# Performance work log

Hardware: AMD Instinct MI355X
Metric: run time of the kernel (lower is better)

Reference implementation:

```python
import jax, jax.numpy as jnp
import numpy as np

D_MODEL = 512
NUM_HEADS = 8
D_K = D_MODEL // NUM_HEADS


def setup_inputs() -> dict:
    key = jax.random.key(0)
    k0, k1, k2, k3, k4 = jax.random.split(key, 5)
    s = 1.0 / np.sqrt(D_MODEL)
    return {
        "x": jax.random.normal(k0, (2, 4096, D_MODEL), dtype=jnp.float32),
        "W_q": jax.random.normal(k1, (D_MODEL, D_MODEL), dtype=jnp.float32) * s,
        "W_k": jax.random.normal(k2, (D_MODEL, D_MODEL), dtype=jnp.float32) * s,
        "W_v": jax.random.normal(k3, (D_MODEL, D_MODEL), dtype=jnp.float32) * s,
        "W_o": jax.random.normal(k4, (D_MODEL, D_MODEL), dtype=jnp.float32) * s,
    }


def reference(x, W_q, W_k, W_v, W_o):
    B, S, _ = x.shape
    # project and split heads: (B, H, S, d_k)
    def split(t):
        return t.reshape(B, S, NUM_HEADS, D_K).transpose(0, 2, 1, 3)
    Q = split(x @ W_q)
    K = split(x @ W_k)
    V = split(x @ W_v)
    scale = jnp.sqrt(jnp.asarray(D_K, dtype=x.dtype))
    logits = jnp.einsum('bhqd,bhkd->bhqk', Q, K) / scale
    attn = jax.nn.softmax(logits, axis=-1)  # dropout is identity at inference
    out = jnp.einsum('bhqk,bhkd->bhqd', attn, V)
    concat = out.transpose(0, 2, 1, 3).reshape(B, S, D_MODEL)
    return concat @ W_o
```

## Files before the change

kernel.cpp:

```cpp
#include <hip/hip_runtime.h>
#include <hip/hip_bf16.h>


#define DMODEL 512
#define SEQ    4096
#define NTOK   8192
#define LDQK   1024

using f32x4 = __attribute__((ext_vector_type(4))) float;
using s16x8 = __attribute__((ext_vector_type(8))) short;
using u16x8 = __attribute__((ext_vector_type(8))) unsigned short;

static __device__ __forceinline__ unsigned short f2bf(float f) {
  union { float f; unsigned u; } v; v.f = f;
  unsigned r = v.u + 0x7fff + ((v.u >> 16) & 1);
  return (unsigned short)(r >> 16);
}

static __device__ __forceinline__ unsigned pack_bf2(float lo, float hi) {
  __hip_bfloat162 t = __float22bfloat162_rn(make_float2(lo, hi));
  union { __hip_bfloat162 b; unsigned u; } c; c.b = t; return c.u;
}

static __device__ __forceinline__ void gll16(const void* g, void* l) {
  __builtin_amdgcn_global_load_lds(
      (const __attribute__((address_space(1))) unsigned int*)g,
      (__attribute__((address_space(3))) unsigned int*)l, 16, 0, 0);
}

__global__ void prep_kernel(const float* __restrict__ x,
                            const float* __restrict__ Wq,
                            const float* __restrict__ Wk,
                            const float* __restrict__ Wv,
                            const float* __restrict__ Wo,
                            unsigned short* __restrict__ xb,
                            unsigned short* __restrict__ Wall, float c2) {
  __shared__ float T[64][65];
  const int bx = blockIdx.x;
  if (bx < 1024) {
    for (int i = bx * 256 + threadIdx.x; i < NTOK * DMODEL / 4; i += 262144) {
      float4 v = ((const float4*)x)[i];
      ushort4 o;
      o.x = f2bf(v.x); o.y = f2bf(v.y); o.z = f2bf(v.z); o.w = f2bf(v.w);
      ((ushort4*)xb)[i] = o;
    }
    return;
  }
  const int t = bx - 1024;
  const int y = t >> 6, sub = t & 63;
  const float* W = (y == 0) ? Wq : (y == 1) ? Wk : (y == 2) ? Wv : Wo;
  const float scale = (y == 0) ? c2 : 1.0f;
  const int tk = (sub & 7) * 64;
  const int tn = (sub >> 3) * 64;
  const int r  = threadIdx.x >> 2;
  const int cq = threadIdx.x & 3;
#pragma unroll
  for (int i = 0; i < 4; ++i) {
    int c = (cq + 4 * i) * 4;
    float4 v = *(const float4*)&W[(size_t)(tk + r) * 512 + tn + c];
    T[r][c + 0] = v.x * scale; T[r][c + 1] = v.y * scale;
    T[r][c + 2] = v.z * scale; T[r][c + 3] = v.w * scale;
  }
  __syncthreads();
  const int n  = threadIdx.x >> 2;
  const int k0 = (threadIdx.x & 3) * 16;
#pragma unroll
  for (int j4 = 0; j4 < 4; ++j4) {
    ushort4 o;
    o.x = f2bf(T[k0 + j4 * 4 + 0][n]);
    o.y = f2bf(T[k0 + j4 * 4 + 1][n]);
    o.z = f2bf(T[k0 + j4 * 4 + 2][n]);
    o.w = f2bf(T[k0 + j4 * 4 + 3][n]);
    *(ushort4*)&Wall[(size_t)y * 262144 + (size_t)(tn + n) * 512 + tk + k0 + j4 * 4] = o;
  }
}

__global__ __launch_bounds__(256, 3) void gemm_qkv(
    const unsigned short* __restrict__ xb,
    const unsigned short* __restrict__ Wall,
    unsigned short* __restrict__ QKb,
    unsigned short* __restrict__ Vtb)
{
  __shared__ unsigned short As[128 * 32];
  __shared__ unsigned short Bs[128 * 32];
  const int by = blockIdx.y;
  const bool vmode = (by >= 8);
  const unsigned short* A  = vmode ? (Wall + 2 * 262144) : xb;
  const unsigned short* Bt = vmode ? xb : Wall;
  const size_t bm = vmode ? (size_t)(by - 8) * 128 : (size_t)blockIdx.x * 128;
  const size_t bn = vmode ? (size_t)blockIdx.x * 128 : (size_t)by * 128;
  const int tid  = threadIdx.x;
  const int wave = tid >> 6, lane = tid & 63;
  const int q4 = lane >> 4, ln = lane & 15;
  const int wm = (wave >> 1) * 64, wn = (wave & 1) * 64;
  f32x4 acc[4][4] = {};
  const int srow = wave * 16 + (lane >> 2);
  const int scol = (lane & 3) * 8;

  const unsigned short* Ag  = A  + (bm + srow)      * 512 + scol;
  const unsigned short* Ag2 = A  + (bm + 64 + srow) * 512 + scol;
  const unsigned short* Bg  = Bt + (bn + srow)      * 512 + scol;
  const unsigned short* Bg2 = Bt + (bn + 64 + srow) * 512 + scol;
  unsigned short* Ad  = As + wave * 512;
  unsigned short* Ad2 = As + 2048 + wave * 512;
  unsigned short* Bd  = Bs + wave * 512;
  unsigned short* Bd2 = Bs + 2048 + wave * 512;

  for (int kt = 0; kt < 512; kt += 32) {
    __syncthreads();
    gll16(Ag + kt,  Ad);
    gll16(Ag2 + kt, Ad2);
    gll16(Bg + kt,  Bd);
    gll16(Bg2 + kt, Bd2);
    __syncthreads();
    s16x8 af[4], bfr[4];
#pragma unroll
    for (int i = 0; i < 4; i++)
      af[i] = *(const s16x8*)(As + (wm + i * 16 + ln) * 32 + q4 * 8);
#pragma unroll
    for (int i = 0; i < 4; i++)
      bfr[i] = *(const s16x8*)(Bs + (wn + i * 16 + ln) * 32 + q4 * 8);
#pragma unroll
    for (int mi = 0; mi < 4; mi++)
#pragma unroll
      for (int ni = 0; ni < 4; ni++)
        acc[mi][ni] = __builtin_amdgcn_mfma_f32_16x16x32_bf16(
            af[mi], bfr[ni], acc[mi][ni], 0, 0, 0);
  }
#pragma unroll
  for (int mi = 0; mi < 4; mi++)
#pragma unroll
    for (int r = 0; r < 4; ++r) {
      size_t row = bm + wm + mi * 16 + q4 * 4 + r;
#pragma unroll
      for (int ni = 0; ni < 4; ni++) {
        size_t col = bn + wn + ni * 16 + ln;
        unsigned short hv = f2bf(acc[mi][ni][r]);
        if (!vmode) {
          QKb[row * 1024 + col] = hv;
        } else {
          int b = (int)(col >> 12), s = (int)(col & 4095);
          int sp = (s & ~63) | (s & 32) | (((s >> 2) & 3) << 3) |
                   (((s >> 4) & 1) << 2) | (s & 3);
          Vtb[(size_t)b * 2097152 + row * 4096 + sp] = hv;
        }
      }
    }
}

__global__ __launch_bounds__(256, 2) void attn_kernel(
    const unsigned short* __restrict__ QK,
    const unsigned short* __restrict__ Vt,
    unsigned short* __restrict__ Oc)
{
  const int bid = blockIdx.x + 32 * (blockIdx.y + 8 * blockIdx.z);
  const int lin = (bid & 7) * 64 + (bid >> 3);
  const int qt = lin & 31, bh = lin >> 5;
  const int h = bh & 7, b = bh >> 3;
  const int tid = threadIdx.x, wave = tid >> 6, lane = tid & 63;
  const int q4 = lane >> 4, ln = lane & 15;
  __shared__ unsigned short Ks[2][64 * 64];
  __shared__ unsigned short Vs[2][64 * 64];
  const size_t rowbase = (size_t)b * SEQ;
  const size_t qrow0   = (size_t)qt * 128 + wave * 32;
  const unsigned short* Kp  = QK + rowbase * LDQK + 512 + h * 64;
  const unsigned short* VTp = Vt + ((size_t)(b * 8 + h) * 64) * SEQ;

  s16x8 qf[2][2];
#pragma unroll
  for (int mf = 0; mf < 2; ++mf) {
    const unsigned short* q = QK + (rowbase + qrow0 + mf * 16 + ln) * LDQK + h * 64;
    qf[mf][0] = *(const s16x8*)(q + q4 * 8);
    qf[mf][1] = *(const s16x8*)(q + 32 + q4 * 8);
  }
  f32x4 o[2][4] = {};
  float lp[2] = {};

  const int srow = tid >> 2;
  const int c32  = (tid & 3) * 32;
  const int swz  = (srow & 7) << 4;
  const int wof0 = srow * 128 + ((c32 +  0) ^ swz);
  const int wof1 = srow * 128 + ((c32 + 16) ^ swz);
  const int rswz = (ln & 7) << 4;

  const unsigned short* kgp = Kp  + (size_t)srow * LDQK + (c32 >> 1);
  const unsigned short* vgp = VTp + (size_t)srow * SEQ + (c32 >> 1);

  u16x8 kr  = *(const u16x8*)kgp;
  u16x8 kr2 = *(const u16x8*)(kgp + 8);
  u16x8 vr  = *(const u16x8*)vgp;
  u16x8 vr2 = *(const u16x8*)(vgp + 8);
  *(u16x8*)((char*)Ks[0] + wof0) = kr;
  *(u16x8*)((char*)Ks[0] + wof1) = kr2;
  *(u16x8*)((char*)Vs[0] + wof0) = vr;
  *(u16x8*)((char*)Vs[0] + wof1) = vr2;
  kgp += (size_t)64 * LDQK;  vgp += 64;
  kr  = *(const u16x8*)kgp;
  kr2 = *(const u16x8*)(kgp + 8);
  vr  = *(const u16x8*)vgp;
  vr2 = *(const u16x8*)(vgp + 8);
  __syncthreads();

  const f32x4 fz = {0.f, 0.f, 0.f, 0.f};

  s16x8 vfp[2][4];
  s16x8 pfp[2][2];

  {
    const char* Kc = (const char*)Ks[0];
    const char* Vc = (const char*)Vs[0];
    f32x4 s4[2][4];
#pragma unroll
    for (int ni = 0; ni < 4; ni++) {
      const char* kb = Kc + (ni * 16 + ln) * 128;
      s16x8 kf0 = *(const s16x8*)(kb + ((q4 * 16)      ^ rswz));
      s16x8 kf1 = *(const s16x8*)(kb + ((q4 * 16 + 64) ^ rswz));
      __builtin_amdgcn_s_setprio(1);
#pragma unroll
      for (int mf = 0; mf < 2; ++mf) {
        f32x4 acc0 = __builtin_amdgcn_mfma_f32_16x16x32_bf16(kf0, qf[mf][0], fz, 0, 0, 0);
        s4[mf][ni] = __builtin_amdgcn_mfma_f32_16x16x32_bf16(kf1, qf[mf][1], acc0, 0, 0, 0);
      }
      __builtin_amdgcn_s_setprio(0);
    }
#pragma unroll
    for (int ks = 0; ks < 2; ++ks)
#pragma unroll
      for (int ni = 0; ni < 4; ni++)
        vfp[ks][ni] = *(const s16x8*)(Vc + (ni * 16 + ln) * 128 +
                                      ((ks * 64 + q4 * 16) ^ rswz));
#pragma unroll
    for (int mf = 0; mf < 2; ++mf) {
      float e[4][4];
#pragma unroll
      for (int ni = 0; ni < 4; ni++)
#pragma unroll
        for (int r = 0; r < 4; ++r)
          e[ni][r] = __builtin_amdgcn_exp2f(s4[mf][ni][r]);
      float t0 = (e[0][0] + e[0][1]) + (e[0][2] + e[0][3]);
      float t1 = (e[1][0] + e[1][1]) + (e[1][2] + e[1][3]);
      float t2 = (e[2][0] + e[2][1]) + (e[2][2] + e[2][3]);
      float t3 = (e[3][0] + e[3][1]) + (e[3][2] + e[3][3]);
      lp[mf] += (t0 + t1) + (t2 + t3);
#pragma unroll
      for (int ks = 0; ks < 2; ++ks) {
        union { s16x8 v; unsigned u[4]; } pu;
        pu.u[0] = pack_bf2(e[2 * ks][0],     e[2 * ks][1]);
        pu.u[1] = pack_bf2(e[2 * ks][2],     e[2 * ks][3]);
        pu.u[2] = pack_bf2(e[2 * ks + 1][0], e[2 * ks + 1][1]);
        pu.u[3] = pack_bf2(e[2 * ks + 1][2], e[2 * ks + 1][3]);
        pfp[mf][ks] = pu.v;
      }
    }
    char* Kn = (char*)Ks[1];
    char* Vn = (char*)Vs[1];
    *(u16x8*)(Kn + wof0) = kr;
    *(u16x8*)(Kn + wof1) = kr2;
    *(u16x8*)(Vn + wof0) = vr;
    *(u16x8*)(Vn + wof1) = vr2;
    kgp += (size_t)64 * LDQK;  vgp += 64;
    kr  = *(const u16x8*)kgp;
    kr2 = *(const u16x8*)(kgp + 8);
    vr  = *(const u16x8*)vgp;
    vr2 = *(const u16x8*)(vgp + 8);
    __syncthreads();
  }

  for (int t = 1; t < 64; ++t) {
    const int cur = t & 1;
    const char* Kc = (const char*)Ks[cur];
    const char* Vc = (const char*)Vs[cur];

    f32x4 s4[2][4];
#pragma unroll
    for (int ni = 0; ni < 4; ni++) {
      const char* kb = Kc + (ni * 16 + ln) * 128;
      s16x8 kf0 = *(const s16x8*)(kb + ((q4 * 16)      ^ rswz));
      s16x8 kf1 = *(const s16x8*)(kb + ((q4 * 16 + 64) ^ rswz));
      __builtin_amdgcn_s_setprio(1);
#pragma unroll
      for (int mf = 0; mf < 2; ++mf) {
        f32x4 acc0 = __builtin_amdgcn_mfma_f32_16x16x32_bf16(kf0, qf[mf][0], fz, 0, 0, 0);
        s4[mf][ni] = __builtin_amdgcn_mfma_f32_16x16x32_bf16(kf1, qf[mf][1], acc0, 0, 0, 0);
      }
      __builtin_amdgcn_s_setprio(0);
    }

#pragma unroll
    for (int ks = 0; ks < 2; ++ks)
#pragma unroll
      for (int ni = 0; ni < 4; ni++)
#pragma unroll
        for (int mf = 0; mf < 2; ++mf)
          o[mf][ni] = __builtin_amdgcn_mfma_f32_16x16x32_bf16(pfp[mf][ks], vfp[ks][ni], o[mf][ni], 0, 0, 0);

    s16x8 vfc[2][4];
#pragma unroll
    for (int ks = 0; ks < 2; ++ks)
#pragma unroll
      for (int ni = 0; ni < 4; ni++)
        vfc[ks][ni] = *(const s16x8*)(Vc + (ni * 16 + ln) * 128 +
                                      ((ks * 64 + q4 * 16) ^ rswz));

    s16x8 pfc[2][2];
#pragma unroll
    for (int mf = 0; mf < 2; ++mf) {
      float e[4][4];
#pragma unroll
      for (int ni = 0; ni < 4; ni++)
#pragma unroll
        for (int r = 0; r < 4; ++r)
          e[ni][r] = __builtin_amdgcn_exp2f(s4[mf][ni][r]);
      float t0 = (e[0][0] + e[0][1]) + (e[0][2] + e[0][3]);
      float t1 = (e[1][0] + e[1][1]) + (e[1][2] + e[1][3]);
      float t2 = (e[2][0] + e[2][1]) + (e[2][2] + e[2][3]);
      float t3 = (e[3][0] + e[3][1]) + (e[3][2] + e[3][3]);
      lp[mf] += (t0 + t1) + (t2 + t3);
#pragma unroll
      for (int ks = 0; ks < 2; ++ks) {
        union { s16x8 v; unsigned u[4]; } pu;
        pu.u[0] = pack_bf2(e[2 * ks][0],     e[2 * ks][1]);
        pu.u[1] = pack_bf2(e[2 * ks][2],     e[2 * ks][3]);
        pu.u[2] = pack_bf2(e[2 * ks + 1][0], e[2 * ks + 1][1]);
        pu.u[3] = pack_bf2(e[2 * ks + 1][2], e[2 * ks + 1][3]);
        pfc[mf][ks] = pu.v;
      }
    }

    if (t + 1 < 64) {
      char* Kn = (char*)Ks[cur ^ 1];
      char* Vn = (char*)Vs[cur ^ 1];
      *(u16x8*)(Kn + wof0) = kr;
      *(u16x8*)(Kn + wof1) = kr2;
      *(u16x8*)(Vn + wof0) = vr;
      *(u16x8*)(Vn + wof1) = vr2;
      if (t + 2 < 64) {
        kgp += (size_t)64 * LDQK;  vgp += 64;
        kr  = *(const u16x8*)kgp;
        kr2 = *(const u16x8*)(kgp + 8);
        vr  = *(const u16x8*)vgp;
        vr2 = *(const u16x8*)(vgp + 8);
      }
    }

#pragma unroll
    for (int ks = 0; ks < 2; ++ks)
#pragma unroll
      for (int ni = 0; ni < 4; ni++)
        vfp[ks][ni] = vfc[ks][ni];
#pragma unroll
    for (int mf = 0; mf < 2; ++mf)
#pragma unroll
      for (int ks = 0; ks < 2; ++ks)
        pfp[mf][ks] = pfc[mf][ks];

    __syncthreads();
  }

  __builtin_amdgcn_s_setprio(1);
#pragma unroll
  for (int ks = 0; ks < 2; ++ks)
#pragma unroll
    for (int ni = 0; ni < 4; ni++)
#pragma unroll
      for (int mf = 0; mf < 2; ++mf)
        o[mf][ni] = __builtin_amdgcn_mfma_f32_16x16x32_bf16(pfp[mf][ks], vfp[ks][ni], o[mf][ni], 0, 0, 0);
  __builtin_amdgcn_s_setprio(0);

#pragma unroll
  for (int mf = 0; mf < 2; ++mf) {
    float l = lp[mf];
    l += __shfl_xor(l, 16, 64);
    l += __shfl_xor(l, 32, 64);
    const float inv = 1.0f / l;
#pragma unroll
    for (int r = 0; r < 4; ++r) {
      const float nv = __shfl(inv, q4 * 4 + r, 64);
      const size_t row = rowbase + qrow0 + mf * 16 + q4 * 4 + r;
#pragma unroll
      for (int ni = 0; ni < 4; ni++)
        Oc[row * 512 + h * 64 + ni * 16 + ln] = f2bf(o[mf][ni][r] * nv);
    }
  }
}

__global__ __launch_bounds__(256, 3) void gemm_out(
    const unsigned short* __restrict__ A,
    const unsigned short* __restrict__ Bt,
    float* __restrict__ C)
{
  __shared__ unsigned short As[128 * 32];
  __shared__ unsigned short Bs[64 * 32];
  const int tid  = threadIdx.x;
  const int wave = tid >> 6, lane = tid & 63;
  const int q4 = lane >> 4, ln = lane & 15;
  const size_t bm = (size_t)blockIdx.x * 128;
  const size_t bn = (size_t)blockIdx.y * 64;
  const int wm = (wave >> 1) * 64, wn = (wave & 1) * 32;
  f32x4 acc[4][2] = {};
  const int srow = wave * 16 + (lane >> 2);
  const int scol = (lane & 3) * 8;

  const unsigned short* Ag  = A  + (bm + srow)      * 512 + scol;
  const unsigned short* Ag2 = A  + (bm + 64 + srow) * 512 + scol;
  const unsigned short* Bg  = Bt + (bn + srow)      * 512 + scol;
  unsigned short* Ad  = As + wave * 512;
  unsigned short* Ad2 = As + 2048 + wave * 512;
  unsigned short* Bd  = Bs + wave * 512;

  for (int kt = 0; kt < 512; kt += 32) {
    __syncthreads();
    gll16(Ag + kt,  Ad);
    gll16(Ag2 + kt, Ad2);
    gll16(Bg + kt,  Bd);
    __syncthreads();
    s16x8 af[4], bfr[2];
#pragma unroll
    for (int i = 0; i < 4; i++)
      af[i] = *(const s16x8*)(As + (wm + i * 16 + ln) * 32 + q4 * 8);
#pragma unroll
    for (int i = 0; i < 2; i++)
      bfr[i] = *(const s16x8*)(Bs + (wn + i * 16 + ln) * 32 + q4 * 8);
#pragma unroll
    for (int mi = 0; mi < 4; mi++)
#pragma unroll
      for (int ni = 0; ni < 2; ni++)
        acc[mi][ni] = __builtin_amdgcn_mfma_f32_16x16x32_bf16(
            af[mi], bfr[ni], acc[mi][ni], 0, 0, 0);
  }
#pragma unroll
  for (int mi = 0; mi < 4; mi++)
#pragma unroll
    for (int r = 0; r < 4; ++r) {
      size_t row = bm + wm + mi * 16 + q4 * 4 + r;
#pragma unroll
      for (int ni = 0; ni < 2; ni++)
        C[row * 512 + bn + wn + ni * 16 + ln] = acc[mi][ni][r];
    }
}

extern "C" void kernel_launch(void* const* d_in, const int* in_sizes, int n_in,
                              void* d_out, int out_size, void* d_ws, size_t ws_size,
                              hipStream_t stream) {
  const float* x  = (const float*)d_in[0];
  const float* Wq = (const float*)d_in[1];
  const float* Wk = (const float*)d_in[2];
  const float* Wv = (const float*)d_in[3];
  const float* Wo = (const float*)d_in[4];

  char* ws = (char*)d_ws;
  unsigned short* xb    = (unsigned short*)(ws);
  unsigned short* Wall  = (unsigned short*)(ws + 8388608);
  unsigned short* QKb   = (unsigned short*)(ws + 10485760);
  unsigned short* Vtb   = (unsigned short*)(ws + 27262976);
  unsigned short* Oc    = (unsigned short*)(ws + 35651584);

  const float C2 = 0.125f * 1.44269504088896f;

  hipLaunchKernelGGL(prep_kernel, dim3(1280), dim3(256), 0, stream,
                     x, Wq, Wk, Wv, Wo, xb, Wall, C2);
  hipLaunchKernelGGL(gemm_qkv, dim3(64, 12), dim3(256), 0, stream,
                     xb, Wall, QKb, Vtb);
  hipLaunchKernelGGL(attn_kernel, dim3(32, 8, 2), dim3(256), 0, stream,
                     QKb, Vtb, Oc);
  hipLaunchKernelGGL(gemm_out, dim3(64, 8), dim3(256), 0, stream,
                     Oc, Wall + 3 * 262144, (float*)d_out);
}
```

Baseline: 185.4 us.

## Stage K/V tiles with direct global-to-LDS loads and compute row sums via MFMA

Replaces the register-staged K/V double buffering (global load to registers, then LDS store) with direct global-to-LDS 16-byte loads issued at the top of each iteration for the next tile. It also drops the scalar exp-sum reduction and the final cross-lane shuffles, instead accumulating softmax denominators with an extra MFMA against a vector of bf16 ones. This aims to cut VGPR pressure and VALU/LDS-store work in the attention loop, at the cost of four extra MFMAs per iteration. The row sums now come from the bf16-rounded probabilities, which matches what is multiplied into V.

```diff
diff --git a/kernel.cpp b/kernel.cpp
--- a/kernel.cpp
+++ b/kernel.cpp
@@ -174,31 +174,31 @@
     qf[mf][1] = *(const s16x8*)(q + 32 + q4 * 8);
   }
   f32x4 o[2][4] = {};
-  float lp[2] = {};
-
-  const int srow = tid >> 2;
-  const int c32  = (tid & 3) * 32;
-  const int swz  = (srow & 7) << 4;
-  const int wof0 = srow * 128 + ((c32 +  0) ^ swz);
-  const int wof1 = srow * 128 + ((c32 + 16) ^ swz);
+  f32x4 ol[2]   = {};
+
+  s16x8 onesf;
+#pragma unroll
+  for (int j = 0; j < 8; ++j) onesf[j] = (short)0x3F80;
+
   const int rswz = (ln & 7) << 4;
 
-  const unsigned short* kgp = Kp  + (size_t)srow * LDQK + (c32 >> 1);
-  const unsigned short* vgp = VTp + (size_t)srow * SEQ + (c32 >> 1);
-
-  u16x8 kr  = *(const u16x8*)kgp;
-  u16x8 kr2 = *(const u16x8*)(kgp + 8);
-  u16x8 vr  = *(const u16x8*)vgp;
-  u16x8 vr2 = *(const u16x8*)(vgp + 8);
-  *(u16x8*)((char*)Ks[0] + wof0) = kr;
-  *(u16x8*)((char*)Ks[0] + wof1) = kr2;
-  *(u16x8*)((char*)Vs[0] + wof0) = vr;
-  *(u16x8*)((char*)Vs[0] + wof1) = vr2;
-  kgp += (size_t)64 * LDQK;  vgp += 64;
-  kr  = *(const u16x8*)kgp;
-  kr2 = *(const u16x8*)(kgp + 8);
-  vr  = *(const u16x8*)vgp;
-  vr2 = *(const u16x8*)(vgp + 8);
+  const int rlo = lane >> 3;
+  const int sb  = (((lane & 7) << 4)) ^ (rlo << 4);
+  const char* kgb = (const char*)Kp  + (size_t)(wave * 16 + rlo) * 2048 + sb;
+  const char* vgb = (const char*)VTp + (size_t)(wave * 16 + rlo) * 8192 + sb;
+
+  auto stage = [&](int tt, int nb) {
+    char* Kd = (char*)Ks[nb] + wave * 2048;
+    char* Vd = (char*)Vs[nb] + wave * 2048;
+    const char* kg = kgb + (size_t)tt * 131072;
+    const char* vg = vgb + (size_t)tt * 128;
+    gll16(kg,         Kd);
+    gll16(kg + 16384, Kd + 1024);
+    gll16(vg,         Vd);
+    gll16(vg + 65536, Vd + 1024);
+  };
+
+  stage(0, 0);
   __syncthreads();
 
   const f32x4 fz = {0.f, 0.f, 0.f, 0.f};
@@ -209,6 +209,7 @@
   {
     const char* Kc = (const char*)Ks[0];
     const char* Vc = (const char*)Vs[0];
+    stage(1, 1);
     f32x4 s4[2][4];
 #pragma unroll
     for (int ni = 0; ni < 4; ni++) {
@@ -237,11 +238,6 @@
 #pragma unroll
         for (int r = 0; r < 4; ++r)
           e[ni][r] = __builtin_amdgcn_exp2f(s4[mf][ni][r]);
-      float t0 = (e[0][0] + e[0][1]) + (e[0][2] + e[0][3]);
-      float t1 = (e[1][0] + e[1][1]) + (e[1][2] + e[1][3]);
-      float t2 = (e[2][0] + e[2][1]) + (e[2][2] + e[2][3]);
-      float t3 = (e[3][0] + e[3][1]) + (e[3][2] + e[3][3]);
-      lp[mf] += (t0 + t1) + (t2 + t3);
 #pragma unroll
       for (int ks = 0; ks < 2; ++ks) {
         union { s16x8 v; unsigned u[4]; } pu;
@@ -252,24 +248,16 @@
         pfp[mf][ks] = pu.v;
       }
     }
-    char* Kn = (char*)Ks[1];
-    char* Vn = (char*)Vs[1];
-    *(u16x8*)(Kn + wof0) = kr;
-    *(u16x8*)(Kn + wof1) = kr2;
-    *(u16x8*)(Vn + wof0) = vr;
-    *(u16x8*)(Vn + wof1) = vr2;
-    kgp += (size_t)64 * LDQK;  vgp += 64;
-    kr  = *(const u16x8*)kgp;
-    kr2 = *(const u16x8*)(kgp + 8);
-    vr  = *(const u16x8*)vgp;
-    vr2 = *(const u16x8*)(vgp + 8);
-    __syncthreads();
-  }
-
+    __syncthreads();
+  }
+
+#pragma unroll 2
   for (int t = 1; t < 64; ++t) {
     const int cur = t & 1;
     const char* Kc = (const char*)Ks[cur];
     const char* Vc = (const char*)Vs[cur];
+
+    if (t + 1 < 64) stage(t + 1, cur ^ 1);
 
     f32x4 s4[2][4];
 #pragma unroll
@@ -293,6 +281,11 @@
 #pragma unroll
         for (int mf = 0; mf < 2; ++mf)
           o[mf][ni] = __builtin_amdgcn_mfma_f32_16x16x32_bf16(pfp[mf][ks], vfp[ks][ni], o[mf][ni], 0, 0, 0);
+#pragma unroll
+    for (int mf = 0; mf < 2; ++mf)
+#pragma unroll
+      for (int ks = 0; ks < 2; ++ks)
+        ol[mf] = __builtin_amdgcn_mfma_f32_16x16x32_bf16(pfp[mf][ks], onesf, ol[mf], 0, 0, 0);
 
     s16x8 vfc[2][4];
 #pragma unroll
@@ -311,11 +304,6 @@
 #pragma unroll
         for (int r = 0; r < 4; ++r)
           e[ni][r] = __builtin_amdgcn_exp2f(s4[mf][ni][r]);
-      float t0 = (e[0][0] + e[0][1]) + (e[0][2] + e[0][3]);
-      float t1 = (e[1][0] + e[1][1]) + (e[1][2] + e[1][3]);
-      float t2 = (e[2][0] + e[2][1]) + (e[2][2] + e[2][3]);
-      float t3 = (e[3][0] + e[3][1]) + (e[3][2] + e[3][3]);
-      lp[mf] += (t0 + t1) + (t2 + t3);
 #pragma unroll
       for (int ks = 0; ks < 2; ++ks) {
         union { s16x8 v; unsigned u[4]; } pu;
@@ -327,22 +315,6 @@
       }
     }
 
-    if (t + 1 < 64) {
-      char* Kn = (char*)Ks[cur ^ 1];
-      char* Vn = (char*)Vs[cur ^ 1];
-      *(u16x8*)(Kn + wof0) = kr;
-      *(u16x8*)(Kn + wof1) = kr2;
-      *(u16x8*)(Vn + wof0) = vr;
-      *(u16x8*)(Vn + wof1) = vr2;
-      if (t + 2 < 64) {
-        kgp += (size_t)64 * LDQK;  vgp += 64;
-        kr  = *(const u16x8*)kgp;
-        kr2 = *(const u16x8*)(kgp + 8);
-        vr  = *(const u16x8*)vgp;
-        vr2 = *(const u16x8*)(vgp + 8);
-      }
-    }
-
 #pragma unroll
     for (int ks = 0; ks < 2; ++ks)
 #pragma unroll
@@ -365,23 +337,23 @@
 #pragma unroll
       for (int mf = 0; mf < 2; ++mf)
         o[mf][ni] = __builtin_amdgcn_mfma_f32_16x16x32_bf16(pfp[mf][ks], vfp[ks][ni], o[mf][ni], 0, 0, 0);
+#pragma unroll
+  for (int mf = 0; mf < 2; ++mf)
+#pragma unroll
+    for (int ks = 0; ks < 2; ++ks)
+      ol[mf] = __builtin_amdgcn_mfma_f32_16x16x32_bf16(pfp[mf][ks], onesf, ol[mf], 0, 0, 0);
   __builtin_amdgcn_s_setprio(0);
 
 #pragma unroll
-  for (int mf = 0; mf < 2; ++mf) {
-    float l = lp[mf];
-    l += __shfl_xor(l, 16, 64);
-    l += __shfl_xor(l, 32, 64);
-    const float inv = 1.0f / l;
+  for (int mf = 0; mf < 2; ++mf)
 #pragma unroll
     for (int r = 0; r < 4; ++r) {
-      const float nv = __shfl(inv, q4 * 4 + r, 64);
+      const float nv = 1.0f / ol[mf][r];
       const size_t row = rowbase + qrow0 + mf * 16 + q4 * 4 + r;
 #pragma unroll
       for (int ni = 0; ni < 4; ni++)
         Oc[row * 512 + h * 64 + ni * 16 + ln] = f2bf(o[mf][ni][r] * nv);
     }
-  }
 }
 
 __global__ __launch_bounds__(256, 3) void gemm_out(
```

Measured after the change: 185.6 us. Within noise of the previous version (+0.1%).
